# Kernel tuning notes

Hardware: AMD Instinct MI355X
Metric: run time of the kernel (lower is better)

The kernel has to match this reference:

```python
import jax, jax.numpy as jnp
import numpy as np

M, N_ATOMS, N_BONDS, MAX_NB = 96, 96, 96, 3
HB = 158        # bond hidden size; linear is 2*HB -> HB
F_ATOM = 133    # unused by forward, present in signature


def _glorot(key, shape):
    fan_in = shape[1]
    return (jax.random.normal(key, shape, jnp.float32) / np.float32(np.sqrt(fan_in)))


def setup_inputs() -> dict:
    key = jax.random.key(0)
    ks = jax.random.split(key, 12)
    return {
        "a2b_": jax.random.randint(ks[0], (M, N_ATOMS, MAX_NB), 1, N_BONDS + 1, dtype=jnp.int32),
        "b2a_": jax.random.randint(ks[1], (M, N_BONDS), 0, N_ATOMS, dtype=jnp.int32),
        "b2revb_": jax.random.randint(ks[2], (M, N_BONDS), 0, N_BONDS, dtype=jnp.int32),
        "f_bonds_": jax.random.normal(ks[3], (M, N_BONDS, HB), jnp.float32),
        "f_atoms_": jax.random.normal(ks[4], (M, N_ATOMS, F_ATOM), jnp.float32),
        "bond_sum_": jnp.zeros((M, HB), jnp.float32),
        "W0": _glorot(ks[5], (HB, 2 * HB)), "b0": jnp.zeros((HB,), jnp.float32),
        "W1": _glorot(ks[6], (110, HB)),    "b1": jnp.zeros((110,), jnp.float32),
        "W2": _glorot(ks[7], (70, 110)),    "b2": jnp.zeros((70,), jnp.float32),
        "W3": _glorot(ks[8], (35, 70)),     "b3": jnp.zeros((35,), jnp.float32),
        "W4": _glorot(ks[9], (1, 35)),      "b4": jnp.zeros((1,), jnp.float32),
    }


def _message_pass(f_bonds, bond_sum, a2b, b2a, b2revb, W0, b0):
    # Faithful sequential replay of the nested python loops for one molecule.
    # f_bonds[c] is overwritten inside the inner loop (torch row view aliases),
    # and bond_sum carries across both loops -> single scan over (c, j) pairs.
    cs = jnp.repeat(jnp.arange(N_BONDS), MAX_NB)
    js = jnp.tile(jnp.arange(MAX_NB), N_BONDS)

    def step(carry, cj):
        fb, bs = carry
        c, j = cj
        d = a2b[b2a[c], j]                      # neighbor bond index (>=1 by construction)
        bs = fb[d - 1] + bs
        bs = bs - fb[b2revb[c]]
        nf = jnp.concatenate([fb[c], bs]) @ W0.T + b0   # 316 -> 158
        fb = fb.at[c].set(nf)
        return (fb, bs), None

    (fb, _), _ = jax.lax.scan(step, (f_bonds, bond_sum), (cs, js))
    return fb.sum(axis=0)                       # [HB]


def reference(a2b_, b2a_, b2revb_, f_bonds_, f_atoms_, bond_sum_,
              W0, b0, W1, b1, W2, b2, W3, b3, W4, b4):
    # f_atoms_ is accepted but never used, exactly as in the source module.
    mp = jax.vmap(_message_pass, in_axes=(0, 0, 0, 0, 0, None, None))(
        f_bonds_, bond_sum_, a2b_, b2a_, b2revb_, W0, b0)   # [M, HB]
    # Dropout layers are identity in eval mode. No activation after layer1 (per source).
    h = mp @ W1.T + b1
    h = jax.nn.relu(h @ W2.T + b2)
    h = jax.nn.relu(h @ W3.T + b3)
    out = h @ W4.T + b4                                    # [M, 1]
    return out.reshape(-1)                                 # cat of [1]-tensors -> [M]
```

## Files before the change

kernel.cpp:

```cpp
#include <hip/hip_runtime.h>

#define NBOND 96
#define HBS 158
#define NSTEP 288
#define NT 320

typedef float f4 __attribute__((ext_vector_type(4)));
#define Z4 ((f4){0.f, 0.f, 0.f, 0.f})
#define MK4(P, B) ((f4){(P)[(B)], (P)[(B)+1], (P)[(B)+2], (P)[(B)+3]})

__global__ __launch_bounds__(NT, 1)
void gcn_mp_kernel(const int* __restrict__ a2b,
                   const int* __restrict__ b2a,
                   const int* __restrict__ b2revb,
                   const float* __restrict__ f_bonds,
                   const float* __restrict__ bond_sum,
                   const float* __restrict__ W0,
                   const float* __restrict__ b0,
                   const float* __restrict__ W1, const float* __restrict__ b1,
                   const float* __restrict__ W2, const float* __restrict__ b2v,
                   const float* __restrict__ W3, const float* __restrict__ b3,
                   const float* __restrict__ W4, const float* __restrict__ b4,
                   float* __restrict__ out)
{
  const int m  = blockIdx.x;
  const int t  = threadIdx.x;
  const int og = t >> 3;
  const int s  = t & 7;

  __shared__ __align__(16) float fb[NBOND * 160];
  __shared__ __align__(16) float xv[2][320];
  __shared__ int sDp[NSTEP];
  __shared__ int sRp[NSTEP];
  __shared__ __align__(16) float mpb[160];
  __shared__ float hb1[112], hb2[72], hb3[40];

  for (int idx = t; idx < NBOND * 160; idx += NT) {
    int r = idx / 160, o = idx - r * 160;
    fb[idx] = (o < HBS) ? f_bonds[(m * NBOND + r) * HBS + o] : 0.f;
  }
  if (t < NSTEP) {
    int i = t, c = i / 3, j = i - 3 * c;
    int a  = b2a[m * NBOND + c];
    int d  = a2b[(m * NBOND + a) * 3 + j] - 1;
    int rv = b2revb[m * NBOND + c];
    int cp = (i == 0) ? -1 : (i - 1) / 3;
    sDp[i] = d  | ((d  == cp) ? 0x10000 : 0);
    sRp[i] = rv | ((rv == cp) ? 0x10000 : 0);
  }

  const int o0 = og * 4;
  const int cb = (s < 4) ? s * 40 : s * 40 - 2;
  const bool edge = (s == 3) || (s == 7);
  const float* P0 = W0 + o0 * (2 * HBS) + cb;
  const float* P1 = W0 + (o0 + 1) * (2 * HBS) + cb;
  const float* P2 = W0 + ((o0 + 2 < HBS) ? o0 + 2 : HBS - 1) * (2 * HBS) + cb;
  const float* P3 = W0 + ((o0 + 3 < HBS) ? o0 + 3 : HBS - 1) * (2 * HBS) + cb;

#define DECLROW(R, P) \
  f4 w##R##0 = MK4(P, 0),  w##R##1 = MK4(P, 4),  w##R##2 = MK4(P, 8),  \
     w##R##3 = MK4(P, 12), w##R##4 = MK4(P, 16), w##R##5 = MK4(P, 20), \
     w##R##6 = MK4(P, 24), w##R##7 = MK4(P, 28), w##R##8 = MK4(P, 32); \
  f4 w##R##9 = (f4){(P)[36], (P)[37], edge ? 0.f : (P)[38], edge ? 0.f : (P)[39]};
  DECLROW(0, P0)
  DECLROW(1, P1)
  DECLROW(2, P2)
  DECLROW(3, P3)
#undef DECLROW
  if (o0 + 2 >= HBS) {
    w20 = Z4; w21 = Z4; w22 = Z4; w23 = Z4; w24 = Z4;
    w25 = Z4; w26 = Z4; w27 = Z4; w28 = Z4; w29 = Z4;
    w30 = Z4; w31 = Z4; w32 = Z4; w33 = Z4; w34 = Z4;
    w35 = Z4; w36 = Z4; w37 = Z4; w38 = Z4; w39 = Z4;
  }
  const float b0r0 = b0[o0];
  const float b0r1 = b0[o0 + 1];
  const float b0r2 = (o0 + 2 < HBS) ? b0[o0 + 2] : 0.f;
  const float b0r3 = (o0 + 3 < HBS) ? b0[o0 + 3] : 0.f;

  asm volatile("" : "+v"(w00), "+v"(w01), "+v"(w02), "+v"(w03), "+v"(w04),
                    "+v"(w05), "+v"(w06), "+v"(w07), "+v"(w08), "+v"(w09));
  asm volatile("" : "+v"(w10), "+v"(w11), "+v"(w12), "+v"(w13), "+v"(w14),
                    "+v"(w15), "+v"(w16), "+v"(w17), "+v"(w18), "+v"(w19));
  asm volatile("" : "+v"(w20), "+v"(w21), "+v"(w22), "+v"(w23), "+v"(w24),
                    "+v"(w25), "+v"(w26), "+v"(w27), "+v"(w28), "+v"(w29));
  asm volatile("" : "+v"(w30), "+v"(w31), "+v"(w32), "+v"(w33), "+v"(w34),
                    "+v"(w35), "+v"(w36), "+v"(w37), "+v"(w38), "+v"(w39));

  __syncthreads();

  if (t < 160) {
    int d0 = sDp[0] & 0xFFFF, r0 = sRp[0] & 0xFFFF;
    xv[0][t] = fb[t];
    float bsv = ((t < HBS) ? bond_sum[m * HBS + t] : 0.f)
              + fb[d0 * 160 + t] - fb[r0 * 160 + t];
    xv[0][160 + t] = bsv;
  }
  __syncthreads();

  float cs0 = 0.f, cs1 = 0.f, cs2 = 0.f, cs3 = 0.f;
  int p = 0;

#pragma unroll 1
  for (int i = 0; i < NSTEP; ++i) {
    const int c  = i / 3;
    const int j  = i - 3 * c;
    const int i1 = i + 1;
    const int c1 = i1 / 3;
    const int j1 = i1 - 3 * c1;
    const bool hn = (i1 < NSTEP);

    const f4* XP = (const f4*)(&xv[p][s * 40]);
    f4 xa = XP[0], xb = XP[1], xc = XP[2], xd = XP[3];

    f4 nxr = Z4;
    float2 dd = make_float2(0.f, 0.f), rr = make_float2(0.f, 0.f), bo = make_float2(0.f, 0.f);
    int aD = 0, aR = 0, e0 = 0;
    if (hn) {
      if (s == 1 && j1 == 0) {
        const float* q = &fb[c1 * 160 + og * 4];
        nxr = (f4){q[0], q[1], q[2], q[3]};
      }
      if (s >= 2 && s <= 3) {
        const int pd = sDp[i1], pr = sRp[i1];
        const int d  = pd & 0xFFFF;  aD = pd >> 16;
        const int rv = pr & 0xFFFF;  aR = pr >> 16;
        e0 = og * 4 + (s - 2) * 2;
        dd = *(const float2*)(&fb[d  * 160 + e0]);
        rr = *(const float2*)(&fb[rv * 160 + e0]);
        bo = *(const float2*)(&xv[p][160 + e0]);
      }
    }

    float a0 = 0.f, a1 = 0.f, a2 = 0.f, a3 = 0.f;
#define QSTEP(Q, XX) \
    a0 = fmaf(w0##Q[0], XX[0], a0); a1 = fmaf(w1##Q[0], XX[0], a1); \
    a2 = fmaf(w2##Q[0], XX[0], a2); a3 = fmaf(w3##Q[0], XX[0], a3); \
    a0 = fmaf(w0##Q[1], XX[1], a0); a1 = fmaf(w1##Q[1], XX[1], a1); \
    a2 = fmaf(w2##Q[1], XX[1], a2); a3 = fmaf(w3##Q[1], XX[1], a3); \
    a0 = fmaf(w0##Q[2], XX[2], a0); a1 = fmaf(w1##Q[2], XX[2], a1); \
    a2 = fmaf(w2##Q[2], XX[2], a2); a3 = fmaf(w3##Q[2], XX[2], a3); \
    a0 = fmaf(w0##Q[3], XX[3], a0); a1 = fmaf(w1##Q[3], XX[3], a1); \
    a2 = fmaf(w2##Q[3], XX[3], a2); a3 = fmaf(w3##Q[3], XX[3], a3);
    QSTEP(0, xa) xa = XP[4];
    QSTEP(1, xb) xb = XP[5];
    QSTEP(2, xc) xc = XP[6];
    QSTEP(3, xd) xd = XP[7];
    QSTEP(4, xa) xa = XP[8];
    QSTEP(5, xb) xb = XP[9];
    QSTEP(6, xc)
    QSTEP(7, xd)
    QSTEP(8, xa)
    QSTEP(9, xb)
#undef QSTEP

    a0 += __shfl_xor(a0, 1); a0 += __shfl_xor(a0, 2); a0 += __shfl_xor(a0, 4);
    a1 += __shfl_xor(a1, 1); a1 += __shfl_xor(a1, 2); a1 += __shfl_xor(a1, 4);
    a2 += __shfl_xor(a2, 1); a2 += __shfl_xor(a2, 2); a2 += __shfl_xor(a2, 4);
    a3 += __shfl_xor(a3, 1); a3 += __shfl_xor(a3, 2); a3 += __shfl_xor(a3, 4);
    a0 += b0r0; a1 += b0r1; a2 += b0r2; a3 += b0r3;

    if (s == 0) {
      *(float4*)(&fb[c * 160 + og * 4]) = make_float4(a0, a1, a2, a3);
    }
    if (hn) {
      if (s == 1) {
        float4 wv = (j1 == 0) ? make_float4(nxr[0], nxr[1], nxr[2], nxr[3])
                              : make_float4(a0, a1, a2, a3);
        *(float4*)(&xv[p ^ 1][og * 4]) = wv;
      }
      if (s >= 2 && s <= 3) {
        float sA = (s == 2) ? a0 : a2;
        float sB = (s == 2) ? a1 : a3;
        float vd0 = aD ? sA : dd.x;
        float vd1 = aD ? sB : dd.y;
        float vr0 = aR ? sA : rr.x;
        float vr1 = aR ? sB : rr.y;
        *(float2*)(&xv[p ^ 1][160 + e0]) =
            make_float2(bo.x + vd0 - vr0, bo.y + vd1 - vr1);
      }
    }
    if (j == 2) { cs0 += a0; cs1 += a1; cs2 += a2; cs3 += a3; }

    p ^= 1;
    __syncthreads();
  }

  if (s == 0) {
    *(float4*)(&mpb[og * 4]) = make_float4(cs0, cs1, cs2, cs3);
  }
  __syncthreads();

  if (t < 110) {
    float acc = b1[t];
    for (int k = 0; k < HBS; ++k) acc = fmaf(mpb[k], W1[t * HBS + k], acc);
    hb1[t] = acc;
  }
  __syncthreads();
  if (t < 70) {
    float acc = b2v[t];
    for (int k = 0; k < 110; ++k) acc = fmaf(hb1[k], W2[t * 110 + k], acc);
    hb2[t] = fmaxf(acc, 0.f);
  }
  __syncthreads();
  if (t < 35) {
    float acc = b3[t];
    for (int k = 0; k < 70; ++k) acc = fmaf(hb2[k], W3[t * 70 + k], acc);
    hb3[t] = fmaxf(acc, 0.f);
  }
  __syncthreads();
  if (t == 0) {
    float acc = b4[0];
    for (int k = 0; k < 35; ++k) acc = fmaf(hb3[k], W4[k], acc);
    out[m] = acc;
  }
}

extern "C" void kernel_launch(void* const* d_in, const int* in_sizes, int n_in,
                              void* d_out, int out_size, void* d_ws, size_t ws_size,
                              hipStream_t stream)
{
  const int*   a2b      = (const int*)d_in[0];
  const int*   b2a      = (const int*)d_in[1];
  const int*   b2revb   = (const int*)d_in[2];
  const float* f_bonds  = (const float*)d_in[3];
  const float* bond_sum = (const float*)d_in[5];
  const float* W0 = (const float*)d_in[6];
  const float* b0 = (const float*)d_in[7];
  const float* W1 = (const float*)d_in[8];
  const float* b1 = (const float*)d_in[9];
  const float* W2 = (const float*)d_in[10];
  const float* b2 = (const float*)d_in[11];
  const float* W3 = (const float*)d_in[12];
  const float* b3 = (const float*)d_in[13];
  const float* W4 = (const float*)d_in[14];
  const float* b4 = (const float*)d_in[15];

  gcn_mp_kernel<<<dim3(96), dim3(NT), 0, stream>>>(
      a2b, b2a, b2revb, f_bonds, bond_sum,
      W0, b0, W1, b1, W2, b2, W3, b3, W4, b4,
      (float*)d_out);
}
```

Measured before the change: 290.2 us.

## Repartition W0 matvec across four waves with five strided output rows per thread

The block shrinks from 320 to 256 threads (five waves to four), so each SIMD now gets one wave instead of one SIMD carrying two on the serial critical path. To cover all 158 outputs, each thread now keeps five W0 rows in registers, strided by 32, rather than four contiguous rows. The fb, xv and mpb reads and writes change to match the strided layout, and the bond-sum update moves to a single lane per group. The cost is more register pressure (about 200 weight VGPRs) and scalar rather than vectorised LDS accesses. A 16 KB volatile LDS pad array is also added with no clear purpose.

```diff
diff --git a/kernel.cpp b/kernel.cpp
--- a/kernel.cpp
+++ b/kernel.cpp
@@ -3,7 +3,7 @@
 #define NBOND 96
 #define HBS 158
 #define NSTEP 288
-#define NT 320
+#define NT 256
 
 typedef float f4 __attribute__((ext_vector_type(4)));
 #define Z4 ((f4){0.f, 0.f, 0.f, 0.f})
@@ -34,13 +34,18 @@
   __shared__ int sRp[NSTEP];
   __shared__ __align__(16) float mpb[160];
   __shared__ float hb1[112], hb2[72], hb3[40];
+  __shared__ float lds_pad[4096];
+  {
+    volatile float* vp = lds_pad;
+    vp[t] = 0.f;
+  }
 
   for (int idx = t; idx < NBOND * 160; idx += NT) {
     int r = idx / 160, o = idx - r * 160;
     fb[idx] = (o < HBS) ? f_bonds[(m * NBOND + r) * HBS + o] : 0.f;
   }
-  if (t < NSTEP) {
-    int i = t, c = i / 3, j = i - 3 * c;
+  for (int i = t; i < NSTEP; i += NT) {
+    int c = i / 3, j = i - 3 * c;
     int a  = b2a[m * NBOND + c];
     int d  = a2b[(m * NBOND + a) * 3 + j] - 1;
     int rv = b2revb[m * NBOND + c];
@@ -49,13 +54,14 @@
     sRp[i] = rv | ((rv == cp) ? 0x10000 : 0);
   }
 
-  const int o0 = og * 4;
   const int cb = (s < 4) ? s * 40 : s * 40 - 2;
   const bool edge = (s == 3) || (s == 7);
-  const float* P0 = W0 + o0 * (2 * HBS) + cb;
-  const float* P1 = W0 + (o0 + 1) * (2 * HBS) + cb;
-  const float* P2 = W0 + ((o0 + 2 < HBS) ? o0 + 2 : HBS - 1) * (2 * HBS) + cb;
-  const float* P3 = W0 + ((o0 + 3 < HBS) ? o0 + 3 : HBS - 1) * (2 * HBS) + cb;
+  const float* P0 = W0 + (og      ) * (2 * HBS) + cb;
+  const float* P1 = W0 + (og + 32 ) * (2 * HBS) + cb;
+  const float* P2 = W0 + (og + 64 ) * (2 * HBS) + cb;
+  const float* P3 = W0 + (og + 96 ) * (2 * HBS) + cb;
+  const int o4 = (og + 128 < HBS) ? og + 128 : HBS - 1;
+  const float* P4 = W0 + o4 * (2 * HBS) + cb;
 
 #define DECLROW(R, P) \
   f4 w##R##0 = MK4(P, 0),  w##R##1 = MK4(P, 4),  w##R##2 = MK4(P, 8),  \
@@ -66,17 +72,17 @@
   DECLROW(1, P1)
   DECLROW(2, P2)
   DECLROW(3, P3)
+  DECLROW(4, P4)
 #undef DECLROW
-  if (o0 + 2 >= HBS) {
-    w20 = Z4; w21 = Z4; w22 = Z4; w23 = Z4; w24 = Z4;
-    w25 = Z4; w26 = Z4; w27 = Z4; w28 = Z4; w29 = Z4;
-    w30 = Z4; w31 = Z4; w32 = Z4; w33 = Z4; w34 = Z4;
-    w35 = Z4; w36 = Z4; w37 = Z4; w38 = Z4; w39 = Z4;
-  }
-  const float b0r0 = b0[o0];
-  const float b0r1 = b0[o0 + 1];
-  const float b0r2 = (o0 + 2 < HBS) ? b0[o0 + 2] : 0.f;
-  const float b0r3 = (o0 + 3 < HBS) ? b0[o0 + 3] : 0.f;
+  if (og + 128 >= HBS) {
+    w40 = Z4; w41 = Z4; w42 = Z4; w43 = Z4; w44 = Z4;
+    w45 = Z4; w46 = Z4; w47 = Z4; w48 = Z4; w49 = Z4;
+  }
+  const float b0r0 = b0[og];
+  const float b0r1 = b0[og + 32];
+  const float b0r2 = b0[og + 64];
+  const float b0r3 = b0[og + 96];
+  const float b0r4 = (og + 128 < HBS) ? b0[og + 128] : 0.f;
 
   asm volatile("" : "+v"(w00), "+v"(w01), "+v"(w02), "+v"(w03), "+v"(w04),
                     "+v"(w05), "+v"(w06), "+v"(w07), "+v"(w08), "+v"(w09));
@@ -86,6 +92,8 @@
                     "+v"(w25), "+v"(w26), "+v"(w27), "+v"(w28), "+v"(w29));
   asm volatile("" : "+v"(w30), "+v"(w31), "+v"(w32), "+v"(w33), "+v"(w34),
                     "+v"(w35), "+v"(w36), "+v"(w37), "+v"(w38), "+v"(w39));
+  asm volatile("" : "+v"(w40), "+v"(w41), "+v"(w42), "+v"(w43), "+v"(w44),
+                    "+v"(w45), "+v"(w46), "+v"(w47), "+v"(w48), "+v"(w49));
 
   __syncthreads();
 
@@ -98,7 +106,7 @@
   }
   __syncthreads();
 
-  float cs0 = 0.f, cs1 = 0.f, cs2 = 0.f, cs3 = 0.f;
+  float cs0 = 0.f, cs1 = 0.f, cs2 = 0.f, cs3 = 0.f, cs4 = 0.f;
   int p = 0;
 
 #pragma unroll 1
@@ -113,35 +121,43 @@
     const f4* XP = (const f4*)(&xv[p][s * 40]);
     f4 xa = XP[0], xb = XP[1], xc = XP[2], xd = XP[3];
 
-    f4 nxr = Z4;
-    float2 dd = make_float2(0.f, 0.f), rr = make_float2(0.f, 0.f), bo = make_float2(0.f, 0.f);
-    int aD = 0, aR = 0, e0 = 0;
+    float nx0 = 0.f, nx1 = 0.f, nx2 = 0.f, nx3 = 0.f, nx4 = 0.f;
+    float dd0 = 0.f, dd1 = 0.f, dd2 = 0.f, dd3 = 0.f, dd4 = 0.f;
+    float rr0 = 0.f, rr1 = 0.f, rr2 = 0.f, rr3 = 0.f, rr4 = 0.f;
+    float bo0 = 0.f, bo1 = 0.f, bo2 = 0.f, bo3 = 0.f, bo4 = 0.f;
+    int aD = 0, aR = 0;
     if (hn) {
       if (s == 1 && j1 == 0) {
-        const float* q = &fb[c1 * 160 + og * 4];
-        nxr = (f4){q[0], q[1], q[2], q[3]};
-      }
-      if (s >= 2 && s <= 3) {
+        const float* q = &fb[c1 * 160 + og];
+        nx0 = q[0]; nx1 = q[32]; nx2 = q[64]; nx3 = q[96]; nx4 = q[128];
+      }
+      if (s == 2) {
         const int pd = sDp[i1], pr = sRp[i1];
         const int d  = pd & 0xFFFF;  aD = pd >> 16;
         const int rv = pr & 0xFFFF;  aR = pr >> 16;
-        e0 = og * 4 + (s - 2) * 2;
-        dd = *(const float2*)(&fb[d  * 160 + e0]);
-        rr = *(const float2*)(&fb[rv * 160 + e0]);
-        bo = *(const float2*)(&xv[p][160 + e0]);
+        const float* qd = &fb[d  * 160 + og];
+        const float* qr = &fb[rv * 160 + og];
+        const float* qb = &xv[p][160 + og];
+        dd0 = qd[0]; dd1 = qd[32]; dd2 = qd[64]; dd3 = qd[96]; dd4 = qd[128];
+        rr0 = qr[0]; rr1 = qr[32]; rr2 = qr[64]; rr3 = qr[96]; rr4 = qr[128];
+        bo0 = qb[0]; bo1 = qb[32]; bo2 = qb[64]; bo3 = qb[96]; bo4 = qb[128];
       }
     }
 
-    float a0 = 0.f, a1 = 0.f, a2 = 0.f, a3 = 0.f;
+    float a0 = 0.f, a1 = 0.f, a2 = 0.f, a3 = 0.f, a4 = 0.f;
 #define QSTEP(Q, XX) \
     a0 = fmaf(w0##Q[0], XX[0], a0); a1 = fmaf(w1##Q[0], XX[0], a1); \
     a2 = fmaf(w2##Q[0], XX[0], a2); a3 = fmaf(w3##Q[0], XX[0], a3); \
+    a4 = fmaf(w4##Q[0], XX[0], a4); \
     a0 = fmaf(w0##Q[1], XX[1], a0); a1 = fmaf(w1##Q[1], XX[1], a1); \
     a2 = fmaf(w2##Q[1], XX[1], a2); a3 = fmaf(w3##Q[1], XX[1], a3); \
+    a4 = fmaf(w4##Q[1], XX[1], a4); \
     a0 = fmaf(w0##Q[2], XX[2], a0); a1 = fmaf(w1##Q[2], XX[2], a1); \
     a2 = fmaf(w2##Q[2], XX[2], a2); a3 = fmaf(w3##Q[2], XX[2], a3); \
+    a4 = fmaf(w4##Q[2], XX[2], a4); \
     a0 = fmaf(w0##Q[3], XX[3], a0); a1 = fmaf(w1##Q[3], XX[3], a1); \
-    a2 = fmaf(w2##Q[3], XX[3], a2); a3 = fmaf(w3##Q[3], XX[3], a3);
+    a2 = fmaf(w2##Q[3], XX[3], a2); a3 = fmaf(w3##Q[3], XX[3], a3); \
+    a4 = fmaf(w4##Q[3], XX[3], a4);
     QSTEP(0, xa) xa = XP[4];
     QSTEP(1, xb) xb = XP[5];
     QSTEP(2, xc) xc = XP[6];
@@ -158,36 +174,41 @@
     a1 += __shfl_xor(a1, 1); a1 += __shfl_xor(a1, 2); a1 += __shfl_xor(a1, 4);
     a2 += __shfl_xor(a2, 1); a2 += __shfl_xor(a2, 2); a2 += __shfl_xor(a2, 4);
     a3 += __shfl_xor(a3, 1); a3 += __shfl_xor(a3, 2); a3 += __shfl_xor(a3, 4);
-    a0 += b0r0; a1 += b0r1; a2 += b0r2; a3 += b0r3;
+    a4 += __shfl_xor(a4, 1); a4 += __shfl_xor(a4, 2); a4 += __shfl_xor(a4, 4);
+    a0 += b0r0; a1 += b0r1; a2 += b0r2; a3 += b0r3; a4 += b0r4;
 
     if (s == 0) {
-      *(float4*)(&fb[c * 160 + og * 4]) = make_float4(a0, a1, a2, a3);
+      float* q = &fb[c * 160 + og];
+      q[0] = a0; q[32] = a1; q[64] = a2; q[96] = a3; q[128] = a4;
     }
     if (hn) {
+      const int pn = p ^ 1;
       if (s == 1) {
-        float4 wv = (j1 == 0) ? make_float4(nxr[0], nxr[1], nxr[2], nxr[3])
-                              : make_float4(a0, a1, a2, a3);
-        *(float4*)(&xv[p ^ 1][og * 4]) = wv;
-      }
-      if (s >= 2 && s <= 3) {
-        float sA = (s == 2) ? a0 : a2;
-        float sB = (s == 2) ? a1 : a3;
-        float vd0 = aD ? sA : dd.x;
-        float vd1 = aD ? sB : dd.y;
-        float vr0 = aR ? sA : rr.x;
-        float vr1 = aR ? sB : rr.y;
-        *(float2*)(&xv[p ^ 1][160 + e0]) =
-            make_float2(bo.x + vd0 - vr0, bo.y + vd1 - vr1);
+        float* q = &xv[pn][og];
+        q[0]   = (j1 == 0) ? nx0 : a0;
+        q[32]  = (j1 == 0) ? nx1 : a1;
+        q[64]  = (j1 == 0) ? nx2 : a2;
+        q[96]  = (j1 == 0) ? nx3 : a3;
+        q[128] = (j1 == 0) ? nx4 : a4;
+      }
+      if (s == 2) {
+        float* q = &xv[pn][160 + og];
+        q[0]   = bo0 + (aD ? a0 : dd0) - (aR ? a0 : rr0);
+        q[32]  = bo1 + (aD ? a1 : dd1) - (aR ? a1 : rr1);
+        q[64]  = bo2 + (aD ? a2 : dd2) - (aR ? a2 : rr2);
+        q[96]  = bo3 + (aD ? a3 : dd3) - (aR ? a3 : rr3);
+        q[128] = bo4 + (aD ? a4 : dd4) - (aR ? a4 : rr4);
       }
     }
-    if (j == 2) { cs0 += a0; cs1 += a1; cs2 += a2; cs3 += a3; }
+    if (j == 2) { cs0 += a0; cs1 += a1; cs2 += a2; cs3 += a3; cs4 += a4; }
 
     p ^= 1;
     __syncthreads();
   }
 
-  if (s == 0) {
-    *(float4*)(&mpb[og * 4]) = make_float4(cs0, cs1, cs2, cs3);
+  if (s == 4) {
+    float* q = &mpb[og];
+    q[0] = cs0; q[32] = cs1; q[64] = cs2; q[96] = cs3; q[128] = cs4;
   }
   __syncthreads();
 
```

New measurement: 343.0 us. 18.2% more time.
